# Optimization experiments

Measured on AMD Instinct MI355X. Metric: run time of the kernel, lower is better.

Reference implementation:

```python
import jax, jax.numpy as jnp
import numpy as np


def setup_inputs() -> dict:
    key = jax.random.key(0)
    k1, k2 = jax.random.split(key)
    B, T, D, E = 4, 4096, 2048, 64
    x = jax.random.normal(k1, (B, T, D), dtype=jnp.float32)
    # nn.Linear default init ~ U(-1/sqrt(D), 1/sqrt(D)); scaled normal is fine for a numeric baseline
    W = jax.random.normal(k2, (D, E), dtype=jnp.float32) * (1.0 / np.sqrt(D))
    b = jnp.zeros((E,), dtype=jnp.float32)
    return {"x": x, "W": W, "b": b}


TOPK = 2


def reference(x, W, b):
    # logits: (B, T, E)
    logits = jnp.einsum("btd,de->bte", x, W) + b
    probs = jax.nn.softmax(logits, axis=-1)
    topk_vals, topk_idx = jax.lax.top_k(probs, TOPK)
    return topk_idx, topk_vals
```

## Files before the change

kernel.cpp:

```cpp
#include <hip/hip_runtime.h>
#include <math.h>


#define D_DIM 2048
#define E_DIM 64
#define M_DIM 16384
#define RM 32

typedef _Float16 half8 __attribute__((ext_vector_type(8)));
typedef float floatx4 __attribute__((ext_vector_type(4)));
typedef unsigned int uint;

__global__ __launch_bounds__(256) void split_w_kernel(
    const float* __restrict__ Wm, _Float16* __restrict__ wsT)
{
    const int tid = threadIdx.x;
    const int n   = tid & 63;
    const int kk0 = tid >> 6;
    const int g   = blockIdx.x;
    #pragma unroll
    for (int r = 0; r < 8; r++) {
        const int kk = kk0 + r * 4;
        const float v = Wm[(size_t)(g * 32 + kk) * E_DIM + n];
        const _Float16 h = (_Float16)v;
        const _Float16 l = (_Float16)((v - (float)h) * 2048.0f);
        const int t = n >> 4, cc = n & 15, qd = kk >> 3, j = kk & 7;
        const size_t base = (size_t)((g * 4 + t) * 2) * 512 + (size_t)(qd * 16 + cc) * 8 + j;
        wsT[base]       = h;
        wsT[base + 512] = l;
    }
}

__global__ __launch_bounds__(256, 2) void router_mfma_kernel(
    const float* __restrict__ x, const _Float16* __restrict__ wsT,
    const float* __restrict__ bias, float* __restrict__ out)
{
    __shared__ float red[4 * RM * 65];

    const int lane = threadIdx.x & 63;
    const int wave = threadIdx.x >> 6;
    const int c    = lane & 15;
    const int quad = lane >> 4;
    const int r0   = blockIdx.x * RM;
    const int kb   = wave * (D_DIM / 4);

    const float* xg0 = x + (size_t)(r0 + c) * D_DIM + kb + quad * 8;
    const float* xg1 = xg0 + (size_t)16 * D_DIM;
    const _Float16* wbase = wsT + (size_t)(wave * 16) * 4096 + (size_t)lane * 8;

    floatx4 accm[2][4] = {};
    floatx4 accl[2][4] = {};

    float4 a0A, a1A, b0A, b1A;
    float4 a0B, a1B, b0B, b1B;
    half8 wh0[4], wl0[4], wh1[4], wl1[4];

    auto loadxA = [&](int u) {
        const int uu = u < 16 ? u : 15;
        a0A = *reinterpret_cast<const float4*>(xg0 + uu * 32);
        a1A = *reinterpret_cast<const float4*>(xg0 + uu * 32 + 4);
        b0A = *reinterpret_cast<const float4*>(xg1 + uu * 32);
        b1A = *reinterpret_cast<const float4*>(xg1 + uu * 32 + 4);
    };
    auto loadxB = [&](int u) {
        const int uu = u < 16 ? u : 15;
        a0B = *reinterpret_cast<const float4*>(xg0 + uu * 32);
        a1B = *reinterpret_cast<const float4*>(xg0 + uu * 32 + 4);
        b0B = *reinterpret_cast<const float4*>(xg1 + uu * 32);
        b1B = *reinterpret_cast<const float4*>(xg1 + uu * 32 + 4);
    };
    auto loadW = [&](int u, half8* wh, half8* wl) {
        const int uu = u < 16 ? u : 15;
        const _Float16* p = wbase + (size_t)uu * 4096;
        #pragma unroll
        for (int t = 0; t < 4; t++) {
            wh[t] = *reinterpret_cast<const half8*>(p + t * 1024);
            wl[t] = *reinterpret_cast<const half8*>(p + t * 1024 + 512);
        }
    };
    auto mkfrag = [&](const float4& u0, const float4& u1, half8& h8, half8& l8) {
        const float f[8] = {u0.x, u0.y, u0.z, u0.w, u1.x, u1.y, u1.z, u1.w};
        uint hq[4], lq[4];
        #pragma unroll
        for (int p = 0; p < 4; p++) {
            const float f0 = f[2 * p], f1 = f[2 * p + 1];
            const float h0 = __uint_as_float(__float_as_uint(f0) & 0xFFFFE000u);
            const float h1 = __uint_as_float(__float_as_uint(f1) & 0xFFFFE000u);
            hq[p] = __builtin_bit_cast(uint, __builtin_amdgcn_cvt_pkrtz(h0, h1));
            lq[p] = __builtin_bit_cast(uint,
                        __builtin_amdgcn_cvt_pkrtz((f0 - h0) * 2048.0f, (f1 - h1) * 2048.0f));
        }
        h8 = __builtin_bit_cast(half8, make_uint4(hq[0], hq[1], hq[2], hq[3]));
        l8 = __builtin_bit_cast(half8, make_uint4(lq[0], lq[1], lq[2], lq[3]));
    };
    auto stepA = [&](const half8* wh, const half8* wl) {
        half8 xh0, xl0, xh1, xl1;
        mkfrag(a0A, a1A, xh0, xl0);
        mkfrag(b0A, b1A, xh1, xl1);
        #pragma unroll
        for (int t = 0; t < 4; t++) {
            accm[0][t] = __builtin_amdgcn_mfma_f32_16x16x32_f16(wh[t], xh0, accm[0][t], 0, 0, 0);
            accl[0][t] = __builtin_amdgcn_mfma_f32_16x16x32_f16(wh[t], xl0, accl[0][t], 0, 0, 0);
            accl[0][t] = __builtin_amdgcn_mfma_f32_16x16x32_f16(wl[t], xh0, accl[0][t], 0, 0, 0);
            accm[1][t] = __builtin_amdgcn_mfma_f32_16x16x32_f16(wh[t], xh1, accm[1][t], 0, 0, 0);
            accl[1][t] = __builtin_amdgcn_mfma_f32_16x16x32_f16(wh[t], xl1, accl[1][t], 0, 0, 0);
            accl[1][t] = __builtin_amdgcn_mfma_f32_16x16x32_f16(wl[t], xh1, accl[1][t], 0, 0, 0);
        }
    };
    auto stepB = [&](const half8* wh, const half8* wl) {
        half8 xh0, xl0, xh1, xl1;
        mkfrag(a0B, a1B, xh0, xl0);
        mkfrag(b0B, b1B, xh1, xl1);
        #pragma unroll
        for (int t = 0; t < 4; t++) {
            accm[0][t] = __builtin_amdgcn_mfma_f32_16x16x32_f16(wh[t], xh0, accm[0][t], 0, 0, 0);
            accl[0][t] = __builtin_amdgcn_mfma_f32_16x16x32_f16(wh[t], xl0, accl[0][t], 0, 0, 0);
            accl[0][t] = __builtin_amdgcn_mfma_f32_16x16x32_f16(wl[t], xh0, accl[0][t], 0, 0, 0);
            accm[1][t] = __builtin_amdgcn_mfma_f32_16x16x32_f16(wh[t], xh1, accm[1][t], 0, 0, 0);
            accl[1][t] = __builtin_amdgcn_mfma_f32_16x16x32_f16(wh[t], xl1, accl[1][t], 0, 0, 0);
            accl[1][t] = __builtin_amdgcn_mfma_f32_16x16x32_f16(wl[t], xh1, accl[1][t], 0, 0, 0);
        }
    };

    loadxA(0);
    loadxB(1);
    loadW(0, wh0, wl0);

    #pragma unroll 1
    for (int u = 0; u < 16; u += 2) {
        loadW(u + 1, wh1, wl1);
        stepA(wh0, wl0);
        loadxA(u + 2);
        loadW(u + 2, wh0, wl0);
        stepB(wh1, wl1);
        loadxB(u + 3);
    }

    const float scale = 1.0f / 2048.0f;
    #pragma unroll
    for (int rg = 0; rg < 2; rg++)
        #pragma unroll
        for (int t = 0; t < 4; t++)
            #pragma unroll
            for (int i = 0; i < 4; i++)
                red[(wave * 32 + rg * 16 + c) * 65 + t * 16 + quad * 4 + i] =
                    accm[rg][t][i] + accl[rg][t][i] * scale;
    __syncthreads();

    if (wave >= 2) return;

    float bvt[4];
    #pragma unroll
    for (int t = 0; t < 4; t++) bvt[t] = bias[c + 16 * t];

    #pragma unroll
    for (int i = 0; i < 4; i++) {
        const int row = wave * 16 + quad * 4 + i;
        float lt[4];
        #pragma unroll
        for (int t = 0; t < 4; t++) {
            const int col = c + 16 * t;
            lt[t] = red[(0 * 32 + row) * 65 + col] + red[(1 * 32 + row) * 65 + col]
                  + red[(2 * 32 + row) * 65 + col] + red[(3 * 32 + row) * 65 + col] + bvt[t];
        }
        const float l0 = lt[0], l1 = lt[1], l2 = lt[2], l3 = lt[3];

        float m = fmaxf(fmaxf(l0, l1), fmaxf(l2, l3));
        #pragma unroll
        for (int off = 1; off < 16; off <<= 1)
            m = fmaxf(m, __shfl_xor(m, off, 64));

        const float e0 = expf(l0 - m), e1 = expf(l1 - m);
        const float e2 = expf(l2 - m), e3 = expf(l3 - m);
        float s = e0 + e1 + e2 + e3;
        #pragma unroll
        for (int off = 1; off < 16; off <<= 1)
            s += __shfl_xor(s, off, 64);

        const float p0 = e0 / s, p1 = e1 / s, p2 = e2 / s, p3 = e3 / s;

        const unsigned long long ka =
            ((unsigned long long)__float_as_uint(p0) << 32) | (unsigned long long)(63 - c);
        const unsigned long long kb_ =
            ((unsigned long long)__float_as_uint(p1) << 32) | (unsigned long long)(47 - c);
        const unsigned long long kc_ =
            ((unsigned long long)__float_as_uint(p2) << 32) | (unsigned long long)(31 - c);
        const unsigned long long kd =
            ((unsigned long long)__float_as_uint(p3) << 32) | (unsigned long long)(15 - c);

        unsigned long long hi1 = ka > kb_ ? ka : kb_, lo1 = ka > kb_ ? kb_ : ka;
        unsigned long long hi2 = kc_ > kd ? kc_ : kd, lo2 = kc_ > kd ? kd : kc_;
        unsigned long long k1 = hi1 > hi2 ? hi1 : hi2;
        unsigned long long mn = hi1 > hi2 ? hi2 : hi1;
        unsigned long long mx = lo1 > lo2 ? lo1 : lo2;
        unsigned long long k2 = mn > mx ? mn : mx;

        #pragma unroll
        for (int off = 1; off < 16; off <<= 1) {
            const unsigned long long o1 = __shfl_xor(k1, off, 64);
            const unsigned long long o2 = __shfl_xor(k2, off, 64);
            const unsigned long long n1 = k1 > o1 ? k1 : o1;
            const unsigned long long w1 = k1 > o1 ? o1 : k1;
            const unsigned long long w2 = k2 > o2 ? k2 : o2;
            k1 = n1;
            k2 = w1 > w2 ? w1 : w2;
        }

        if (c == 0) {
            const int gr = r0 + row;
            out[gr * 2 + 0] = (float)(63 - (int)(k1 & 0xFFFFFFFFull));
            out[gr * 2 + 1] = (float)(63 - (int)(k2 & 0xFFFFFFFFull));
            out[M_DIM * 2 + gr * 2 + 0] = __uint_as_float((unsigned)(k1 >> 32));
            out[M_DIM * 2 + gr * 2 + 1] = __uint_as_float((unsigned)(k2 >> 32));
        }
    }
}

extern "C" void kernel_launch(void* const* d_in, const int* in_sizes, int n_in,
                              void* d_out, int out_size, void* d_ws, size_t ws_size,
                              hipStream_t stream) {
    const float* x  = (const float*)d_in[0];
    const float* Wm = (const float*)d_in[1];
    const float* b  = (const float*)d_in[2];
    float* out = (float*)d_out;
    _Float16* wsT = (_Float16*)d_ws;

    split_w_kernel<<<dim3(64), dim3(256), 0, stream>>>(Wm, wsT);
    router_mfma_kernel<<<dim3(M_DIM / RM), dim3(256), 0, stream>>>(x, wsT, b, out);
}
```

Baseline: 219.0 us.

## Split router GEMM work across waves by expert half and K half with 16-row blocks

```diff
diff --git a/kernel.cpp b/kernel.cpp
--- a/kernel.cpp
+++ b/kernel.cpp
@@ -5,7 +5,7 @@
 #define D_DIM 2048
 #define E_DIM 64
 #define M_DIM 16384
-#define RM 32
+#define RM 16
 
 typedef _Float16 half8 __attribute__((ext_vector_type(8)));
 typedef float floatx4 __attribute__((ext_vector_type(4)));
@@ -31,52 +31,42 @@
     }
 }
 
-__global__ __launch_bounds__(256, 2) void router_mfma_kernel(
+__global__ __launch_bounds__(256, 4) void router_mfma_kernel(
     const float* __restrict__ x, const _Float16* __restrict__ wsT,
     const float* __restrict__ bias, float* __restrict__ out)
 {
-    __shared__ float red[4 * RM * 65];
+    __shared__ float red[2 * RM * 65];
 
     const int lane = threadIdx.x & 63;
     const int wave = threadIdx.x >> 6;
+    const int ew   = wave & 1;
+    const int kw   = wave >> 1;
     const int c    = lane & 15;
     const int quad = lane >> 4;
     const int r0   = blockIdx.x * RM;
-    const int kb   = wave * (D_DIM / 4);
-
-    const float* xg0 = x + (size_t)(r0 + c) * D_DIM + kb + quad * 8;
-    const float* xg1 = xg0 + (size_t)16 * D_DIM;
-    const _Float16* wbase = wsT + (size_t)(wave * 16) * 4096 + (size_t)lane * 8;
-
-    floatx4 accm[2][4] = {};
-    floatx4 accl[2][4] = {};
-
-    float4 a0A, a1A, b0A, b1A;
-    float4 a0B, a1B, b0B, b1B;
-    half8 wh0[4], wl0[4], wh1[4], wl1[4];
-
-    auto loadxA = [&](int u) {
-        const int uu = u < 16 ? u : 15;
-        a0A = *reinterpret_cast<const float4*>(xg0 + uu * 32);
-        a1A = *reinterpret_cast<const float4*>(xg0 + uu * 32 + 4);
-        b0A = *reinterpret_cast<const float4*>(xg1 + uu * 32);
-        b1A = *reinterpret_cast<const float4*>(xg1 + uu * 32 + 4);
-    };
-    auto loadxB = [&](int u) {
-        const int uu = u < 16 ? u : 15;
-        a0B = *reinterpret_cast<const float4*>(xg0 + uu * 32);
-        a1B = *reinterpret_cast<const float4*>(xg0 + uu * 32 + 4);
-        b0B = *reinterpret_cast<const float4*>(xg1 + uu * 32);
-        b1B = *reinterpret_cast<const float4*>(xg1 + uu * 32 + 4);
+
+    const float* xg = x + (size_t)(r0 + c) * D_DIM + kw * 1024 + quad * 8;
+    const _Float16* wbase = wsT + (size_t)(kw * 32) * 4096
+                                + (size_t)(ew * 2) * 1024 + (size_t)lane * 8;
+
+    floatx4 accm[2] = {};
+    floatx4 accl[2] = {};
+
+    float4 q0[2], q1[2], q2[2], q3[2];
+    half8 whA[2], wlA[2], whB[2], wlB[2];
+
+    auto loadx = [&](int u, float4* q) {
+        const int uu = u < 32 ? u : 31;
+        q[0] = *reinterpret_cast<const float4*>(xg + uu * 32);
+        q[1] = *reinterpret_cast<const float4*>(xg + uu * 32 + 4);
     };
     auto loadW = [&](int u, half8* wh, half8* wl) {
-        const int uu = u < 16 ? u : 15;
+        const int uu = u < 32 ? u : 31;
         const _Float16* p = wbase + (size_t)uu * 4096;
-        #pragma unroll
-        for (int t = 0; t < 4; t++) {
-            wh[t] = *reinterpret_cast<const half8*>(p + t * 1024);
-            wl[t] = *reinterpret_cast<const half8*>(p + t * 1024 + 512);
-        }
+        wh[0] = *reinterpret_cast<const half8*>(p);
+        wl[0] = *reinterpret_cast<const half8*>(p + 512);
+        wh[1] = *reinterpret_cast<const half8*>(p + 1024);
+        wl[1] = *reinterpret_cast<const half8*>(p + 1024 + 512);
     };
     auto mkfrag = [&](const float4& u0, const float4& u1, half8& h8, half8& l8) {
         const float f[8] = {u0.x, u0.y, u0.z, u0.w, u1.x, u1.y, u1.z, u1.w};
@@ -93,61 +83,42 @@
         h8 = __builtin_bit_cast(half8, make_uint4(hq[0], hq[1], hq[2], hq[3]));
         l8 = __builtin_bit_cast(half8, make_uint4(lq[0], lq[1], lq[2], lq[3]));
     };
-    auto stepA = [&](const half8* wh, const half8* wl) {
-        half8 xh0, xl0, xh1, xl1;
-        mkfrag(a0A, a1A, xh0, xl0);
-        mkfrag(b0A, b1A, xh1, xl1);
-        #pragma unroll
-        for (int t = 0; t < 4; t++) {
-            accm[0][t] = __builtin_amdgcn_mfma_f32_16x16x32_f16(wh[t], xh0, accm[0][t], 0, 0, 0);
-            accl[0][t] = __builtin_amdgcn_mfma_f32_16x16x32_f16(wh[t], xl0, accl[0][t], 0, 0, 0);
-            accl[0][t] = __builtin_amdgcn_mfma_f32_16x16x32_f16(wl[t], xh0, accl[0][t], 0, 0, 0);
-            accm[1][t] = __builtin_amdgcn_mfma_f32_16x16x32_f16(wh[t], xh1, accm[1][t], 0, 0, 0);
-            accl[1][t] = __builtin_amdgcn_mfma_f32_16x16x32_f16(wh[t], xl1, accl[1][t], 0, 0, 0);
-            accl[1][t] = __builtin_amdgcn_mfma_f32_16x16x32_f16(wl[t], xh1, accl[1][t], 0, 0, 0);
-        }
-    };
-    auto stepB = [&](const half8* wh, const half8* wl) {
-        half8 xh0, xl0, xh1, xl1;
-        mkfrag(a0B, a1B, xh0, xl0);
-        mkfrag(b0B, b1B, xh1, xl1);
-        #pragma unroll
-        for (int t = 0; t < 4; t++) {
-            accm[0][t] = __builtin_amdgcn_mfma_f32_16x16x32_f16(wh[t], xh0, accm[0][t], 0, 0, 0);
-            accl[0][t] = __builtin_amdgcn_mfma_f32_16x16x32_f16(wh[t], xl0, accl[0][t], 0, 0, 0);
-            accl[0][t] = __builtin_amdgcn_mfma_f32_16x16x32_f16(wl[t], xh0, accl[0][t], 0, 0, 0);
-            accm[1][t] = __builtin_amdgcn_mfma_f32_16x16x32_f16(wh[t], xh1, accm[1][t], 0, 0, 0);
-            accl[1][t] = __builtin_amdgcn_mfma_f32_16x16x32_f16(wh[t], xl1, accl[1][t], 0, 0, 0);
-            accl[1][t] = __builtin_amdgcn_mfma_f32_16x16x32_f16(wl[t], xh1, accl[1][t], 0, 0, 0);
-        }
-    };
-
-    loadxA(0);
-    loadxB(1);
-    loadW(0, wh0, wl0);
+    auto step = [&](const float4* q, const half8* wh, const half8* wl) {
+        half8 xh, xl;
+        mkfrag(q[0], q[1], xh, xl);
+        #pragma unroll
+        for (int t = 0; t < 2; t++) {
+            accm[t] = __builtin_amdgcn_mfma_f32_16x16x32_f16(wh[t], xh, accm[t], 0, 0, 0);
+            accl[t] = __builtin_amdgcn_mfma_f32_16x16x32_f16(wh[t], xl, accl[t], 0, 0, 0);
+            accl[t] = __builtin_amdgcn_mfma_f32_16x16x32_f16(wl[t], xh, accl[t], 0, 0, 0);
+        }
+    };
+
+    loadx(0, q0); loadx(1, q1); loadx(2, q2); loadx(3, q3);
+    loadW(0, whA, wlA);
 
     #pragma unroll 1
-    for (int u = 0; u < 16; u += 2) {
-        loadW(u + 1, wh1, wl1);
-        stepA(wh0, wl0);
-        loadxA(u + 2);
-        loadW(u + 2, wh0, wl0);
-        stepB(wh1, wl1);
-        loadxB(u + 3);
+    for (int u = 0; u < 32; u += 4) {
+        loadW(u + 1, whB, wlB);
+        step(q0, whA, wlA);  loadx(u + 4, q0);
+        loadW(u + 2, whA, wlA);
+        step(q1, whB, wlB);  loadx(u + 5, q1);
+        loadW(u + 3, whB, wlB);
+        step(q2, whA, wlA);  loadx(u + 6, q2);
+        loadW(u + 4, whA, wlA);
+        step(q3, whB, wlB);  loadx(u + 7, q3);
     }
 
     const float scale = 1.0f / 2048.0f;
     #pragma unroll
-    for (int rg = 0; rg < 2; rg++)
-        #pragma unroll
-        for (int t = 0; t < 4; t++)
-            #pragma unroll
-            for (int i = 0; i < 4; i++)
-                red[(wave * 32 + rg * 16 + c) * 65 + t * 16 + quad * 4 + i] =
-                    accm[rg][t][i] + accl[rg][t][i] * scale;
+    for (int t = 0; t < 2; t++)
+        #pragma unroll
+        for (int i = 0; i < 4; i++)
+            red[(kw * 16 + c) * 65 + (ew * 2 + t) * 16 + quad * 4 + i] =
+                accm[t][i] + accl[t][i] * scale;
     __syncthreads();
 
-    if (wave >= 2) return;
+    if (wave != 0) return;
 
     float bvt[4];
     #pragma unroll
@@ -155,13 +126,12 @@
 
     #pragma unroll
     for (int i = 0; i < 4; i++) {
-        const int row = wave * 16 + quad * 4 + i;
+        const int row = quad * 4 + i;
         float lt[4];
         #pragma unroll
         for (int t = 0; t < 4; t++) {
             const int col = c + 16 * t;
-            lt[t] = red[(0 * 32 + row) * 65 + col] + red[(1 * 32 + row) * 65 + col]
-                  + red[(2 * 32 + row) * 65 + col] + red[(3 * 32 + row) * 65 + col] + bvt[t];
+            lt[t] = red[(0 * 16 + row) * 65 + col] + red[(1 * 16 + row) * 65 + col] + bvt[t];
         }
         const float l0 = lt[0], l1 = lt[1], l2 = lt[2], l3 = lt[3];
 
```

Result: slower. 268.3 us (+22.5%).
